# Kernel tuning notes

Hardware: AMD Instinct MI355X
Metric: run time of the kernel (lower is better)

The kernel has to match this reference:

```python
import jax, jax.numpy as jnp
import numpy as np

E = 200000
T = 1000000
D = 128          # embed_dim
NB = 20          # n_basis (use_sh=False -> SimpleMLPAngleExpansion)


def setup_inputs() -> dict:
    key = jax.random.key(0)
    ks = jax.random.split(key, 16)
    s = lambda fan_in: 1.0 / np.sqrt(fan_in)
    return {
        "edge_attr": jax.random.normal(ks[0], (E, D), dtype=jnp.float32),
        "three_body_indices": jax.random.randint(ks[1], (T, 3), 0, 50000),
        "three_body_edge_indices": jax.random.randint(ks[2], (T, 2), 0, E),
        "edge_vectors": jax.random.normal(ks[3], (E, 3), dtype=jnp.float32),
        # SimpleMLPAngleExpansion: (len_ij, len_ik, cos) -> n_basis via 2-layer MLP
        "A1": jax.random.uniform(ks[4], (3, NB), jnp.float32, -s(3), s(3)),
        "ab1": jnp.zeros((NB,), jnp.float32),
        "A2": jax.random.uniform(ks[5], (NB, NB), jnp.float32, -s(NB), s(NB)),
        "ab2": jnp.zeros((NB,), jnp.float32),
        # phi_3b: Linear(2D+NB, D) -> SiLU -> Linear(D, D)
        "W1": jax.random.uniform(ks[6], (2 * D + NB, D), jnp.float32, -s(2 * D + NB), s(2 * D + NB)),
        "b1": jnp.zeros((D,), jnp.float32),
        "W2": jax.random.uniform(ks[7], (D, D), jnp.float32, -s(D), s(D)),
        "b2": jnp.zeros((D,), jnp.float32),
        # update_edge: Linear(D, D)
        "Wu": jax.random.uniform(ks[8], (D, D), jnp.float32, -s(D), s(D)),
        "bu": jnp.zeros((D,), jnp.float32),
    }


def reference(edge_attr, three_body_indices, three_body_edge_indices, edge_vectors,
              A1, ab1, A2, ab2, W1, b1, W2, b2, Wu, bu):
    e_ij = three_body_edge_indices[:, 0]
    e_ik = three_body_edge_indices[:, 1]
    vec_ij = -edge_vectors[e_ij]          # (T, 3)
    vec_ik = -edge_vectors[e_ik]          # (T, 3)
    len_ij = jnp.clip(jnp.linalg.norm(vec_ij, axis=1, keepdims=True), 1e-6)
    len_ik = jnp.clip(jnp.linalg.norm(vec_ik, axis=1, keepdims=True), 1e-6)
    cos = jnp.clip(jnp.sum(vec_ij * vec_ik, axis=1, keepdims=True) / (len_ij * len_ik), -1.0, 1.0)
    # angle expansion (SimpleMLPAngleExpansion): small MLP on geometric scalars
    f = jnp.concatenate([len_ij, len_ik, cos], axis=-1)       # (T, 3)
    angle_feats = jax.nn.silu(f @ A1 + ab1) @ A2 + ab2         # (T, NB)
    h_3b = jnp.concatenate([edge_attr[e_ij], edge_attr[e_ik], angle_feats], axis=-1)  # (T, 2D+NB)
    m_ijk = jax.nn.silu(h_3b @ W1 + b1) @ W2 + b2              # (T, D)
    delta = jax.ops.segment_sum(m_ijk, e_ij, num_segments=edge_attr.shape[0])  # (E, D)
    return delta @ Wu + bu
```

## Files before the change

### kernel.cpp

```cpp
#include <hip/hip_runtime.h>
#include <stdint.h>

#define D_ 128
#define NB_ 20
#define SCAN_B 1024
#define SEG_BLOCKS 2048
#define NWAVES (SEG_BLOCKS * 256 / 64)

typedef __bf16 bf16x8 __attribute__((ext_vector_type(8)));
typedef float f32x4 __attribute__((ext_vector_type(4)));
typedef float f32x2 __attribute__((ext_vector_type(2)));

__device__ __forceinline__ float silu_f(float x) {
  return x * __builtin_amdgcn_rcpf(1.0f + __expf(-x));
}
__device__ __forceinline__ f32x2 silu2(f32x2 x) {
  return (f32x2){silu_f(x.x), silu_f(x.y)};
}
__device__ __forceinline__ f32x2 fsplat(float x) { return (f32x2){x, x}; }

__device__ __forceinline__ float bf2f(unsigned short u) {
  return __uint_as_float(((unsigned int)u) << 16);
}
__device__ __forceinline__ unsigned short f2bf(float f) {
  unsigned int x = __float_as_uint(f);
  return (unsigned short)((x + 0x7fffu + ((x >> 16) & 1u)) >> 16);
}

__global__ __launch_bounds__(256) void prep_kernel(
    const float* __restrict__ A2, const float* __restrict__ ab2,
    const float* __restrict__ W1, const float* __restrict__ b1,
    const float* __restrict__ W2, const float* __restrict__ Wu,
    const float* __restrict__ b2,
    float* __restrict__ Mfold, float* __restrict__ b1p,
    unsigned short* __restrict__ W2uT, float* __restrict__ c2,
    unsigned short* __restrict__ W1T) {
  int tid = blockIdx.x * blockDim.x + threadIdx.x;
  if (tid < 21 * D_) {
    int r = tid >> 7, c = tid & (D_ - 1);
    if (r < NB_) {
      float acc = 0.f;
      for (int j = 0; j < NB_; ++j) acc += A2[r * NB_ + j] * W1[(2 * D_ + j) * D_ + c];
      Mfold[r * D_ + c] = acc;
    } else {
      float acc = b1[c];
      for (int j = 0; j < NB_; ++j) acc += ab2[j] * W1[(2 * D_ + j) * D_ + c];
      b1p[c] = acc;
    }
  } else if (tid < 2688 + 16384) {
    int i = tid - 2688;
    int n = i >> 7, k = i & 127;
    float acc = 0.f;
    for (int m = 0; m < D_; ++m) acc += W2[k * D_ + m] * Wu[m * D_ + n];
    W2uT[i] = f2bf(acc);
  } else if (tid < 19072 + 128) {
    int n = tid - 19072;
    float acc = 0.f;
    for (int m = 0; m < D_; ++m) acc += b2[m] * Wu[m * D_ + n];
    c2[n] = acc;
  } else if (tid < 19200 + 32768) {
    int i = tid - 19200;
    int r = i >> 7, k = i & 127;
    int half = r >> 7, n = r & 127;
    W1T[i] = f2bf(W1[(size_t)(half * 128 + k) * D_ + n]);
  }
}

__global__ __launch_bounds__(256) void pq_mfma(const float* __restrict__ edge_attr,
                                               const unsigned short* __restrict__ W1T,
                                               unsigned short* __restrict__ P,
                                               unsigned short* __restrict__ Q, int E) {
  const int lane = threadIdx.x & 63;
  const int wave = threadIdx.x >> 6;
  const int e0 = (blockIdx.x * 4 + wave) * 16;
  if (e0 >= E) return;
  const int row = lane & 15;
  const int quad = lane >> 4;
  int e = e0 + row; if (e >= E) e = E - 1;

  union { bf16x8 v; unsigned short u[8]; } afr[4];
  const float* arow = edge_attr + (size_t)e * D_ + quad * 8;
#pragma unroll
  for (int kt = 0; kt < 4; ++kt) {
    float4 f0 = *(const float4*)(arow + kt * 32);
    float4 f1 = *(const float4*)(arow + kt * 32 + 4);
    afr[kt].u[0] = f2bf(f0.x); afr[kt].u[1] = f2bf(f0.y);
    afr[kt].u[2] = f2bf(f0.z); afr[kt].u[3] = f2bf(f0.w);
    afr[kt].u[4] = f2bf(f1.x); afr[kt].u[5] = f2bf(f1.y);
    afr[kt].u[6] = f2bf(f1.z); afr[kt].u[7] = f2bf(f1.w);
  }
#pragma unroll
  for (int half = 0; half < 2; ++half) {
    unsigned short* Obase = half ? Q : P;
#pragma unroll
    for (int nt = 0; nt < 8; ++nt) {
      const unsigned short* wrow =
          W1T + ((size_t)(half * 128 + nt * 16 + row)) * 128 + quad * 8;
      f32x4 acc = {0.f, 0.f, 0.f, 0.f};
#pragma unroll
      for (int kt = 0; kt < 4; ++kt) {
        bf16x8 bfr = *(const bf16x8*)(wrow + kt * 32);
        acc = __builtin_amdgcn_mfma_f32_16x16x32_bf16(afr[kt].v, bfr, acc, 0, 0, 0);
      }
      int n = nt * 16 + row;
#pragma unroll
      for (int i = 0; i < 4; ++i) {
        int er = e0 + quad * 4 + i;
        if (er < E) Obase[(size_t)er * D_ + n] = f2bf(acc[i]);
      }
    }
  }
}

__global__ void hist_kernel(const int* __restrict__ tbe, int* __restrict__ cnt, int T_) {
  int t = blockIdx.x * blockDim.x + threadIdx.x;
  if (t < T_) atomicAdd(&cnt[((const int2*)tbe)[t].x], 1);
}

__global__ __launch_bounds__(SCAN_B) void scan1_kernel(const int* __restrict__ cnt,
                                                       int* __restrict__ pre,
                                                       int* __restrict__ bsum, int E) {
  __shared__ int lds[SCAN_B];
  int tid = threadIdx.x, i = blockIdx.x * SCAN_B + tid;
  int v = (i < E) ? cnt[i] : 0;
  lds[tid] = v;
  __syncthreads();
  for (int d = 1; d < SCAN_B; d <<= 1) {
    int add = (tid >= d) ? lds[tid - d] : 0;
    __syncthreads();
    lds[tid] += add;
    __syncthreads();
  }
  if (i < E) pre[i] = lds[tid] - v;
  if (tid == SCAN_B - 1) bsum[blockIdx.x] = lds[tid];
}

__global__ void scan2_kernel(int* __restrict__ bsum, int nb) {
  __shared__ int lds[256];
  int tid = threadIdx.x;
  int v = (tid < nb) ? bsum[tid] : 0;
  lds[tid] = v;
  __syncthreads();
  for (int d = 1; d < 256; d <<= 1) {
    int add = (tid >= d) ? lds[tid - d] : 0;
    __syncthreads();
    lds[tid] += add;
    __syncthreads();
  }
  if (tid < nb) bsum[tid] = lds[tid] - v;
}

__global__ __launch_bounds__(SCAN_B) void scan3_kernel(const int* __restrict__ pre,
                                                       const int* __restrict__ bsum,
                                                       int* __restrict__ offs,
                                                       int* __restrict__ cursor, int E, int T_) {
  int i = blockIdx.x * SCAN_B + threadIdx.x;
  if (i < E) {
    int o = pre[i] + bsum[blockIdx.x];
    offs[i] = o;
    cursor[i] = o;
  }
  if (i == 0) offs[E] = T_;
}

__global__ __launch_bounds__(256) void wfill_kernel(const int* __restrict__ offs,
                                                    int* __restrict__ wstart,
                                                    int E, int T_, int NW) {
  int e = blockIdx.x * blockDim.x + threadIdx.x;
  if (e >= E) return;
  unsigned long long a = (unsigned long long)offs[e] * (unsigned long long)NW;
  unsigned long long b = (unsigned long long)offs[e + 1] * (unsigned long long)NW;
  int w_lo = (int)((a + T_ - 1) / (unsigned long long)T_);
  int w_hi = (int)((b + T_ - 1) / (unsigned long long)T_);
  for (int w = w_lo; w < w_hi; ++w) wstart[w] = e;
}

__global__ void scatter_kernel(const int* __restrict__ tbe, int* __restrict__ cursor,
                               int2* __restrict__ seik2, int T_) {
  int t = blockIdx.x * blockDim.x + threadIdx.x;
  if (t >= T_) return;
  int2 v = ((const int2*)tbe)[t];
  int pos = atomicAdd(&cursor[v.x], 1);
  seik2[pos] = make_int2(v.y, v.x);
}

__global__ __launch_bounds__(256) void geom_kernel(const int2* __restrict__ seik2,
                                                   const float* __restrict__ edge_vectors,
                                                   const float* __restrict__ A1,
                                                   const float* __restrict__ ab1,
                                                   float* __restrict__ gT, int T_) {
  int t = blockIdx.x * blockDim.x + threadIdx.x;
  if (t >= T_) return;
  int2 s = seik2[t];
  const float* vj = edge_vectors + 3 * (size_t)s.y;
  const float* vk = edge_vectors + 3 * (size_t)s.x;
  float jx = vj[0], jy = vj[1], jz = vj[2];
  float kx = vk[0], ky = vk[1], kz = vk[2];
  float lij = fmaxf(__builtin_amdgcn_sqrtf(jx * jx + jy * jy + jz * jz), 1e-6f);
  float lik = fmaxf(__builtin_amdgcn_sqrtf(kx * kx + ky * ky + kz * kz), 1e-6f);
  float cosv = (jx * kx + jy * ky + jz * kz) * __builtin_amdgcn_rcpf(lij * lik);
  cosv = fminf(fmaxf(cosv, -1.f), 1.f);
  union { float4 v4[5]; float f[NB_]; } gr;
#pragma unroll
  for (int k = 0; k < NB_; ++k)
    gr.f[k] = silu_f(lij * A1[k] + lik * A1[NB_ + k] + cosv * A1[2 * NB_ + k] + ab1[k]);
  float4* gp = (float4*)(gT + (size_t)t * NB_);
#pragma unroll
  for (int i = 0; i < 5; ++i) gp[i] = gr.v4[i];
}

struct G5 { float4 a, b, c, d, e; };

__device__ __forceinline__ G5 loadG(const char* __restrict__ gc, int t) {
  const float4* p = (const float4*)(
      gc + 80u * (unsigned)__builtin_amdgcn_readfirstlane(t));
  G5 g;
  g.a = p[0]; g.b = p[1]; g.c = p[2]; g.d = p[3]; g.e = p[4];
  return g;
}

__device__ __forceinline__ void body_acc(f32x2& acc, const f32x2 base,
                                         const G5& G, ushort2 qq,
                                         const f32x2* __restrict__ m) {
  const float* Gf = (const float*)&G;
  f32x2 u = base + (f32x2){bf2f(qq.x), bf2f(qq.y)};
  f32x2 ub = fsplat(0.f);
#pragma unroll
  for (int k = 0; k < NB_; k += 2) {
    u  += fsplat(Gf[k])     * m[k];
    ub += fsplat(Gf[k + 1]) * m[k + 1];
  }
  u += ub;
  acc += silu2(u);
}

__global__ __launch_bounds__(256, 6) void seg_kernel(
    const int* __restrict__ offs, const int2* __restrict__ seik2,
    const float* __restrict__ gT,
    const float* __restrict__ Mfold, const float* __restrict__ b1p,
    const unsigned short* __restrict__ P, const unsigned short* __restrict__ Q,
    const int* __restrict__ wstart,
    char* __restrict__ s_out, int E, int NW) {
  const int lane = threadIdx.x & 63;
  const int w = __builtin_amdgcn_readfirstlane(
      (int)((blockIdx.x * blockDim.x + threadIdx.x) >> 6));
  if (w >= NW) return;

  f32x2 m[NB_];
#pragma unroll
  for (int k = 0; k < NB_; ++k) {
    float2 t2 = *(const float2*)(Mfold + k * D_ + 2 * lane);
    m[k] = (f32x2){t2.x, t2.y};
  }
  const float2 bbt = *(const float2*)(b1p + 2 * lane);
  const f32x2 bb = (f32x2){bbt.x, bbt.y};

  int es = (w == 0) ? 0 : wstart[w];
  int ee = (w == NW - 1) ? E : wstart[w + 1];
  if (es >= ee) return;

  const char* Qc = (const char*)Q;
  const char* Pc = (const char*)P;
  const char* gc = (const char*)gT;
  const unsigned loff = (unsigned)lane * 4u;

  int e = es;
  int t = offs[es];
  const int tend = offs[ee];
  int nxt = offs[es + 1];

  ushort2 pp = *(const ushort2*)(Pc + ((unsigned)e << 8) + loff);
  int epn = (e + 1 < E) ? e + 1 : E - 1;
  ushort2 ppn = *(const ushort2*)(Pc + ((unsigned)epn << 8) + loff);
  f32x2 base = (f32x2){bf2f(pp.x), bf2f(pp.y)} + bb;
  f32x2 acc = (f32x2){0.f, 0.f};

  if (t < tend) {
    int ek0 = seik2[t].x, ek1 = seik2[t + 1].x, ek2 = seik2[t + 2].x, ek3 = seik2[t + 3].x;
    ushort2 q0 = *(const ushort2*)(Qc + ((unsigned)ek0 << 8) + loff);
    ushort2 q1 = *(const ushort2*)(Qc + ((unsigned)ek1 << 8) + loff);
    ushort2 q2 = *(const ushort2*)(Qc + ((unsigned)ek2 << 8) + loff);
    ushort2 q3 = *(const ushort2*)(Qc + ((unsigned)ek3 << 8) + loff);
    int ekA = seik2[t + 4].x, ekB = seik2[t + 5].x, ekC = seik2[t + 6].x, ekD = seik2[t + 7].x;
    G5 Ga = loadG(gc, t);
    G5 Gb = loadG(gc, t + 1);

    while (t < tend) {
      while (t == nxt) {
        *(ushort2*)(s_out + ((size_t)e << 9) + loff) =
            make_ushort2(f2bf(acc.x), f2bf(acc.y));
        acc = (f32x2){0.f, 0.f};
        ++e;
        nxt = offs[e + 1];
        base = (f32x2){bf2f(ppn.x), bf2f(ppn.y)} + bb;
        int ep = (e + 1 < E) ? e + 1 : E - 1;
        ppn = *(const ushort2*)(Pc + ((unsigned)ep << 8) + loff);
      }
      body_acc(acc, base, Ga, q0, m);
      q0 = q1; q1 = q2; q2 = q3;
      q3 = *(const ushort2*)(Qc + ((unsigned)ekA << 8) + loff);
      ekA = ekB; ekB = ekC; ekC = ekD;
      ekD = seik2[__builtin_amdgcn_readfirstlane(t + 8)].x;
      Ga = loadG(gc, t + 2);
      ++t;
      if (t >= tend) break;
      while (t == nxt) {
        *(ushort2*)(s_out + ((size_t)e << 9) + loff) =
            make_ushort2(f2bf(acc.x), f2bf(acc.y));
        acc = (f32x2){0.f, 0.f};
        ++e;
        nxt = offs[e + 1];
        base = (f32x2){bf2f(ppn.x), bf2f(ppn.y)} + bb;
        int ep = (e + 1 < E) ? e + 1 : E - 1;
        ppn = *(const ushort2*)(Pc + ((unsigned)ep << 8) + loff);
      }
      body_acc(acc, base, Gb, q0, m);
      q0 = q1; q1 = q2; q2 = q3;
      q3 = *(const ushort2*)(Qc + ((unsigned)ekA << 8) + loff);
      ekA = ekB; ekB = ekC; ekC = ekD;
      ekD = seik2[__builtin_amdgcn_readfirstlane(t + 8)].x;
      Gb = loadG(gc, t + 2);
      ++t;
    }
  }
  while (e < ee) {
    *(ushort2*)(s_out + ((size_t)e << 9) + loff) =
        make_ushort2(f2bf(acc.x), f2bf(acc.y));
    acc = (f32x2){0.f, 0.f};
    ++e;
  }
}

__global__ __launch_bounds__(256) void out_mfma(float* __restrict__ io,
                                                const unsigned short* __restrict__ W2uT,
                                                const float* __restrict__ c2,
                                                const float* __restrict__ bu,
                                                const int* __restrict__ cnt, int E) {
  const int lane = threadIdx.x & 63;
  const int wave = threadIdx.x >> 6;
  const int e0 = (blockIdx.x * 4 + wave) * 16;
  if (e0 >= E) return;
  const int row = lane & 15;
  const int quad = lane >> 4;
  int e = e0 + row; if (e >= E) e = E - 1;

  bf16x8 afr[4];
  const char* arow = (const char*)io + ((size_t)e << 9) + quad * 16;
#pragma unroll
  for (int kt = 0; kt < 4; ++kt)
    afr[kt] = *(const bf16x8*)(arow + kt * 64);

  float nf[4];
#pragma unroll
  for (int i = 0; i < 4; ++i) {
    int er = e0 + quad * 4 + i;
    nf[i] = (float)cnt[(er < E) ? er : (E - 1)];
  }
#pragma unroll
  for (int nt = 0; nt < 8; ++nt) {
    const unsigned short* wrow = W2uT + ((size_t)(nt * 16 + row)) * 128 + quad * 8;
    f32x4 acc = {0.f, 0.f, 0.f, 0.f};
#pragma unroll
    for (int kt = 0; kt < 4; ++kt) {
      bf16x8 bfr = *(const bf16x8*)(wrow + kt * 32);
      acc = __builtin_amdgcn_mfma_f32_16x16x32_bf16(afr[kt], bfr, acc, 0, 0, 0);
    }
    int n = nt * 16 + row;
    float c2n = c2[n], bun = bu[n];
#pragma unroll
    for (int i = 0; i < 4; ++i) {
      int er = e0 + quad * 4 + i;
      if (er < E) io[(size_t)er * D_ + n] = acc[i] + nf[i] * c2n + bun;
    }
  }
}

extern "C" void kernel_launch(void* const* d_in, const int* in_sizes, int n_in,
                              void* d_out, int out_size, void* d_ws, size_t ws_size,
                              hipStream_t stream) {
  const float* edge_attr    = (const float*)d_in[0];
  const int*   tbe          = (const int*)d_in[2];
  const float* edge_vectors = (const float*)d_in[3];
  const float* A1  = (const float*)d_in[4];
  const float* ab1 = (const float*)d_in[5];
  const float* A2  = (const float*)d_in[6];
  const float* ab2 = (const float*)d_in[7];
  const float* W1  = (const float*)d_in[8];
  const float* b1  = (const float*)d_in[9];
  const float* W2  = (const float*)d_in[10];
  const float* b2  = (const float*)d_in[11];
  const float* Wu  = (const float*)d_in[12];
  const float* bu  = (const float*)d_in[13];
  const int E = in_sizes[0] / D_;
  const int T = in_sizes[2] / 2;
  float* out = (float*)d_out;

  char* w = (char*)d_ws;
  auto carve = [&](size_t bytes) -> char* {
    char* p = w;
    w += (bytes + 255) & ~(size_t)255;
    return p;
  };
  unsigned short* P = (unsigned short*)carve((size_t)E * D_ * 2);
  unsigned short* Q = (unsigned short*)carve((size_t)E * D_ * 2);
  float* gT   = (float*)carve(((size_t)T + 8) * NB_ * 4);
  int2* seik2 = (int2*)carve(((size_t)T + 8) * 8);
  int* cnt    = (int*)carve((size_t)E * 4);
  int* pre    = (int*)carve((size_t)E * 4);
  int* offs   = (int*)carve((size_t)(E + 1) * 4);
  int* cursor = (int*)carve((size_t)E * 4);
  int* bsum   = (int*)carve(1024 * 4);
  int* wstart = (int*)carve((size_t)NWAVES * 4);
  float* Mfold = (float*)carve(NB_ * D_ * 4);
  float* b1p   = (float*)carve(D_ * 4);
  unsigned short* W2uT = (unsigned short*)carve(D_ * D_ * 2);
  float* c2    = (float*)carve(D_ * 4);
  unsigned short* W1T = (unsigned short*)carve(256 * 128 * 2);

  const int nb_scan = (E + SCAN_B - 1) / SCAN_B;

  hipMemsetAsync(cnt, 0, (size_t)E * 4, stream);
  hipMemsetAsync(seik2 + T, 0, 8 * 8, stream);

  prep_kernel<<<(51968 + 255) / 256, 256, 0, stream>>>(A2, ab2, W1, b1, W2, Wu, b2,
                                                       Mfold, b1p, W2uT, c2, W1T);
  pq_mfma<<<(E + 63) / 64, 256, 0, stream>>>(edge_attr, W1T, P, Q, E);

  hist_kernel<<<(T + 255) / 256, 256, 0, stream>>>(tbe, cnt, T);
  scan1_kernel<<<nb_scan, SCAN_B, 0, stream>>>(cnt, pre, bsum, E);
  scan2_kernel<<<1, 256, 0, stream>>>(bsum, nb_scan);
  scan3_kernel<<<nb_scan, SCAN_B, 0, stream>>>(pre, bsum, offs, cursor, E, T);
  wfill_kernel<<<(E + 255) / 256, 256, 0, stream>>>(offs, wstart, E, T, NWAVES);
  scatter_kernel<<<(T + 255) / 256, 256, 0, stream>>>(tbe, cursor, seik2, T);
  geom_kernel<<<(T + 255) / 256, 256, 0, stream>>>(seik2, edge_vectors, A1, ab1, gT, T);

  seg_kernel<<<SEG_BLOCKS, 256, 0, stream>>>(offs, seik2, gT, Mfold, b1p, P, Q,
                                             wstart, (char*)out, E, NWAVES);
  out_mfma<<<(E + 63) / 64, 256, 0, stream>>>(out, W2uT, c2, bu, cnt, E);
}
```

Measured before the change: 686.8 us.

## Add nontemporal loads/stores on streaming buffers and fuse wfill into scan3

Marks streamed data (edge_attr reads, P writes and reads, gT writes and reads, segment output and final output) as nontemporal so they are less likely to evict the randomly gathered Q rows from cache. Merges the wave-start fill into the scan3 kernel and moves the seik2 padding memset into it, removing one kernel launch and one memset. It also loads bf16 pairs as 32-bit words, unpacked with shifts and masks. Nontemporal hints may hurt if the data they mark is reused before eviction.

```diff
diff --git a/kernel.cpp b/kernel.cpp
--- a/kernel.cpp
+++ b/kernel.cpp
@@ -19,12 +19,15 @@
 }
 __device__ __forceinline__ f32x2 fsplat(float x) { return (f32x2){x, x}; }
 
-__device__ __forceinline__ float bf2f(unsigned short u) {
-  return __uint_as_float(((unsigned int)u) << 16);
-}
 __device__ __forceinline__ unsigned short f2bf(float f) {
   unsigned int x = __float_as_uint(f);
   return (unsigned short)((x + 0x7fffu + ((x >> 16) & 1u)) >> 16);
+}
+__device__ __forceinline__ f32x2 bfpair(unsigned u) {
+  return (f32x2){__uint_as_float(u << 16), __uint_as_float(u & 0xffff0000u)};
+}
+__device__ __forceinline__ unsigned packbf(f32x2 v) {
+  return ((unsigned)f2bf(v.y) << 16) | (unsigned)f2bf(v.x);
 }
 
 __global__ __launch_bounds__(256) void prep_kernel(
@@ -82,12 +85,12 @@
   const float* arow = edge_attr + (size_t)e * D_ + quad * 8;
 #pragma unroll
   for (int kt = 0; kt < 4; ++kt) {
-    float4 f0 = *(const float4*)(arow + kt * 32);
-    float4 f1 = *(const float4*)(arow + kt * 32 + 4);
-    afr[kt].u[0] = f2bf(f0.x); afr[kt].u[1] = f2bf(f0.y);
-    afr[kt].u[2] = f2bf(f0.z); afr[kt].u[3] = f2bf(f0.w);
-    afr[kt].u[4] = f2bf(f1.x); afr[kt].u[5] = f2bf(f1.y);
-    afr[kt].u[6] = f2bf(f1.z); afr[kt].u[7] = f2bf(f1.w);
+    f32x4 f0 = __builtin_nontemporal_load((const f32x4*)(arow + kt * 32));
+    f32x4 f1 = __builtin_nontemporal_load((const f32x4*)(arow + kt * 32 + 4));
+    afr[kt].u[0] = f2bf(f0[0]); afr[kt].u[1] = f2bf(f0[1]);
+    afr[kt].u[2] = f2bf(f0[2]); afr[kt].u[3] = f2bf(f0[3]);
+    afr[kt].u[4] = f2bf(f1[0]); afr[kt].u[5] = f2bf(f1[1]);
+    afr[kt].u[6] = f2bf(f1[2]); afr[kt].u[7] = f2bf(f1[3]);
   }
 #pragma unroll
   for (int half = 0; half < 2; ++half) {
@@ -106,7 +109,12 @@
 #pragma unroll
       for (int i = 0; i < 4; ++i) {
         int er = e0 + quad * 4 + i;
-        if (er < E) Obase[(size_t)er * D_ + n] = f2bf(acc[i]);
+        if (er < E) {
+          if (half == 0)
+            __builtin_nontemporal_store(f2bf(acc[i]), &Obase[(size_t)er * D_ + n]);
+          else
+            Obase[(size_t)er * D_ + n] = f2bf(acc[i]);
+        }
       }
     }
   }
@@ -150,29 +158,25 @@
   if (tid < nb) bsum[tid] = lds[tid] - v;
 }
 
-__global__ __launch_bounds__(SCAN_B) void scan3_kernel(const int* __restrict__ pre,
-                                                       const int* __restrict__ bsum,
-                                                       int* __restrict__ offs,
-                                                       int* __restrict__ cursor, int E, int T_) {
+__global__ __launch_bounds__(SCAN_B) void scan3_wfill(
+    const int* __restrict__ pre, const int* __restrict__ bsum,
+    int* __restrict__ offs, int* __restrict__ cursor,
+    int2* __restrict__ seik2, int* __restrict__ wstart,
+    int E, int T_, int NW) {
   int i = blockIdx.x * SCAN_B + threadIdx.x;
   if (i < E) {
     int o = pre[i] + bsum[blockIdx.x];
     offs[i] = o;
     cursor[i] = o;
+    int onext = (i + 1 < E) ? (pre[i + 1] + bsum[(i + 1) >> 10]) : T_;
+    unsigned long long a = (unsigned long long)o * (unsigned long long)NW;
+    unsigned long long b = (unsigned long long)onext * (unsigned long long)NW;
+    int w_lo = (int)((a + T_ - 1) / (unsigned long long)T_);
+    int w_hi = (int)((b + T_ - 1) / (unsigned long long)T_);
+    for (int w = w_lo; w < w_hi; ++w) wstart[w] = i;
   }
   if (i == 0) offs[E] = T_;
-}
-
-__global__ __launch_bounds__(256) void wfill_kernel(const int* __restrict__ offs,
-                                                    int* __restrict__ wstart,
-                                                    int E, int T_, int NW) {
-  int e = blockIdx.x * blockDim.x + threadIdx.x;
-  if (e >= E) return;
-  unsigned long long a = (unsigned long long)offs[e] * (unsigned long long)NW;
-  unsigned long long b = (unsigned long long)offs[e + 1] * (unsigned long long)NW;
-  int w_lo = (int)((a + T_ - 1) / (unsigned long long)T_);
-  int w_hi = (int)((b + T_ - 1) / (unsigned long long)T_);
-  for (int w = w_lo; w < w_hi; ++w) wstart[w] = e;
+  if (i < 8) seik2[T_ + i] = make_int2(0, 0);
 }
 
 __global__ void scatter_kernel(const int* __restrict__ tbe, int* __restrict__ cursor,
@@ -200,30 +204,34 @@
   float lik = fmaxf(__builtin_amdgcn_sqrtf(kx * kx + ky * ky + kz * kz), 1e-6f);
   float cosv = (jx * kx + jy * ky + jz * kz) * __builtin_amdgcn_rcpf(lij * lik);
   cosv = fminf(fmaxf(cosv, -1.f), 1.f);
-  union { float4 v4[5]; float f[NB_]; } gr;
+  union { f32x4 v4[5]; float f[NB_]; } gr;
 #pragma unroll
   for (int k = 0; k < NB_; ++k)
     gr.f[k] = silu_f(lij * A1[k] + lik * A1[NB_ + k] + cosv * A1[2 * NB_ + k] + ab1[k]);
-  float4* gp = (float4*)(gT + (size_t)t * NB_);
-#pragma unroll
-  for (int i = 0; i < 5; ++i) gp[i] = gr.v4[i];
-}
-
-struct G5 { float4 a, b, c, d, e; };
+  f32x4* gp = (f32x4*)(gT + (size_t)t * NB_);
+#pragma unroll
+  for (int i = 0; i < 5; ++i) __builtin_nontemporal_store(gr.v4[i], gp + i);
+}
+
+struct G5 { f32x4 a, b, c, d, e; };
 
 __device__ __forceinline__ G5 loadG(const char* __restrict__ gc, int t) {
-  const float4* p = (const float4*)(
+  const f32x4* p = (const f32x4*)(
       gc + 80u * (unsigned)__builtin_amdgcn_readfirstlane(t));
   G5 g;
-  g.a = p[0]; g.b = p[1]; g.c = p[2]; g.d = p[3]; g.e = p[4];
+  g.a = __builtin_nontemporal_load(p);
+  g.b = __builtin_nontemporal_load(p + 1);
+  g.c = __builtin_nontemporal_load(p + 2);
+  g.d = __builtin_nontemporal_load(p + 3);
+  g.e = __builtin_nontemporal_load(p + 4);
   return g;
 }
 
 __device__ __forceinline__ void body_acc(f32x2& acc, const f32x2 base,
-                                         const G5& G, ushort2 qq,
+                                         const G5& G, unsigned qw,
                                          const f32x2* __restrict__ m) {
   const float* Gf = (const float*)&G;
-  f32x2 u = base + (f32x2){bf2f(qq.x), bf2f(qq.y)};
+  f32x2 u = base + bfpair(qw);
   f32x2 ub = fsplat(0.f);
 #pragma unroll
   for (int k = 0; k < NB_; k += 2) {
@@ -269,54 +277,58 @@
   const int tend = offs[ee];
   int nxt = offs[es + 1];
 
-  ushort2 pp = *(const ushort2*)(Pc + ((unsigned)e << 8) + loff);
+  unsigned pp = __builtin_nontemporal_load(
+      (const unsigned*)(Pc + ((unsigned)e << 8) + loff));
   int epn = (e + 1 < E) ? e + 1 : E - 1;
-  ushort2 ppn = *(const ushort2*)(Pc + ((unsigned)epn << 8) + loff);
-  f32x2 base = (f32x2){bf2f(pp.x), bf2f(pp.y)} + bb;
+  unsigned ppn = __builtin_nontemporal_load(
+      (const unsigned*)(Pc + ((unsigned)epn << 8) + loff));
+  f32x2 base = bfpair(pp) + bb;
   f32x2 acc = (f32x2){0.f, 0.f};
 
   if (t < tend) {
     int ek0 = seik2[t].x, ek1 = seik2[t + 1].x, ek2 = seik2[t + 2].x, ek3 = seik2[t + 3].x;
-    ushort2 q0 = *(const ushort2*)(Qc + ((unsigned)ek0 << 8) + loff);
-    ushort2 q1 = *(const ushort2*)(Qc + ((unsigned)ek1 << 8) + loff);
-    ushort2 q2 = *(const ushort2*)(Qc + ((unsigned)ek2 << 8) + loff);
-    ushort2 q3 = *(const ushort2*)(Qc + ((unsigned)ek3 << 8) + loff);
+    unsigned q0 = *(const unsigned*)(Qc + ((unsigned)ek0 << 8) + loff);
+    unsigned q1 = *(const unsigned*)(Qc + ((unsigned)ek1 << 8) + loff);
+    unsigned q2 = *(const unsigned*)(Qc + ((unsigned)ek2 << 8) + loff);
+    unsigned q3 = *(const unsigned*)(Qc + ((unsigned)ek3 << 8) + loff);
     int ekA = seik2[t + 4].x, ekB = seik2[t + 5].x, ekC = seik2[t + 6].x, ekD = seik2[t + 7].x;
     G5 Ga = loadG(gc, t);
     G5 Gb = loadG(gc, t + 1);
 
     while (t < tend) {
       while (t == nxt) {
-        *(ushort2*)(s_out + ((size_t)e << 9) + loff) =
-            make_ushort2(f2bf(acc.x), f2bf(acc.y));
+        __builtin_nontemporal_store(
+            packbf(acc), (unsigned*)(s_out + ((size_t)e << 9) + loff));
         acc = (f32x2){0.f, 0.f};
         ++e;
         nxt = offs[e + 1];
-        base = (f32x2){bf2f(ppn.x), bf2f(ppn.y)} + bb;
+        base = bfpair(ppn) + bb;
         int ep = (e + 1 < E) ? e + 1 : E - 1;
-        ppn = *(const ushort2*)(Pc + ((unsigned)ep << 8) + loff);
+        ppn = __builtin_nontemporal_load(
+            (const unsigned*)(Pc + ((unsigned)ep << 8) + loff));
       }
       body_acc(acc, base, Ga, q0, m);
       q0 = q1; q1 = q2; q2 = q3;
-      q3 = *(const ushort2*)(Qc + ((unsigned)ekA << 8) + loff);
+      q3 = *(const unsigned*)(Qc + ((unsigned)ekA << 8) + loff);
       ekA = ekB; ekB = ekC; ekC = ekD;
       ekD = seik2[__builtin_amdgcn_readfirstlane(t + 8)].x;
       Ga = loadG(gc, t + 2);
       ++t;
       if (t >= tend) break;
       while (t == nxt) {
-        *(ushort2*)(s_out + ((size_t)e << 9) + loff) =
-            make_ushort2(f2bf(acc.x), f2bf(acc.y));
+        __builtin_nontemporal_store(
+            packbf(acc), (unsigned*)(s_out + ((size_t)e << 9) + loff));
         acc = (f32x2){0.f, 0.f};
         ++e;
         nxt = offs[e + 1];
-        base = (f32x2){bf2f(ppn.x), bf2f(ppn.y)} + bb;
+        base = bfpair(ppn) + bb;
         int ep = (e + 1 < E) ? e + 1 : E - 1;
-        ppn = *(const ushort2*)(Pc + ((unsigned)ep << 8) + loff);
+        ppn = __builtin_nontemporal_load(
+            (const unsigned*)(Pc + ((unsigned)ep << 8) + loff));
       }
       body_acc(acc, base, Gb, q0, m);
       q0 = q1; q1 = q2; q2 = q3;
-      q3 = *(const ushort2*)(Qc + ((unsigned)ekA << 8) + loff);
+      q3 = *(const unsigned*)(Qc + ((unsigned)ekA << 8) + loff);
       ekA = ekB; ekB = ekC; ekC = ekD;
       ekD = seik2[__builtin_amdgcn_readfirstlane(t + 8)].x;
       Gb = loadG(gc, t + 2);
@@ -324,8 +336,8 @@
     }
   }
   while (e < ee) {
-    *(ushort2*)(s_out + ((size_t)e << 9) + loff) =
-        make_ushort2(f2bf(acc.x), f2bf(acc.y));
+    __builtin_nontemporal_store(
+        packbf(acc), (unsigned*)(s_out + ((size_t)e << 9) + loff));
     acc = (f32x2){0.f, 0.f};
     ++e;
   }
@@ -348,7 +360,7 @@
   const char* arow = (const char*)io + ((size_t)e << 9) + quad * 16;
 #pragma unroll
   for (int kt = 0; kt < 4; ++kt)
-    afr[kt] = *(const bf16x8*)(arow + kt * 64);
+    afr[kt] = __builtin_nontemporal_load((const bf16x8*)(arow + kt * 64));
 
   float nf[4];
 #pragma unroll
@@ -370,7 +382,9 @@
 #pragma unroll
     for (int i = 0; i < 4; ++i) {
       int er = e0 + quad * 4 + i;
-      if (er < E) io[(size_t)er * D_ + n] = acc[i] + nf[i] * c2n + bun;
+      if (er < E)
+        __builtin_nontemporal_store(acc[i] + nf[i] * c2n + bun,
+                                    &io[(size_t)er * D_ + n]);
     }
   }
 }
@@ -420,7 +434,6 @@
   const int nb_scan = (E + SCAN_B - 1) / SCAN_B;
 
   hipMemsetAsync(cnt, 0, (size_t)E * 4, stream);
-  hipMemsetAsync(seik2 + T, 0, 8 * 8, stream);
 
   prep_kernel<<<(51968 + 255) / 256, 256, 0, stream>>>(A2, ab2, W1, b1, W2, Wu, b2,
                                                        Mfold, b1p, W2uT, c2, W1T);
@@ -429,8 +442,8 @@
   hist_kernel<<<(T + 255) / 256, 256, 0, stream>>>(tbe, cnt, T);
   scan1_kernel<<<nb_scan, SCAN_B, 0, stream>>>(cnt, pre, bsum, E);
   scan2_kernel<<<1, 256, 0, stream>>>(bsum, nb_scan);
-  scan3_kernel<<<nb_scan, SCAN_B, 0, stream>>>(pre, bsum, offs, cursor, E, T);
-  wfill_kernel<<<(E + 255) / 256, 256, 0, stream>>>(offs, wstart, E, T, NWAVES);
+  scan3_wfill<<<nb_scan, SCAN_B, 0, stream>>>(pre, bsum, offs, cursor, seik2,
+                                              wstart, E, T, NWAVES);
   scatter_kernel<<<(T + 255) / 256, 256, 0, stream>>>(tbe, cursor, seik2, T);
   geom_kernel<<<(T + 255) / 256, 256, 0, stream>>>(seik2, edge_vectors, A1, ab1, gT, T);
 
```

After: 809.0 us. 17.8% more time.
